# Kernel optimization log

Measured on AMD Instinct MI355X. Metric: run time of the kernel, lower is better.

The kernel has to match this reference:

```python
import jax, jax.numpy as jnp
import numpy as np

T, B, OBS, H, A = 512, 64, 512, 1024, 18


def setup_inputs() -> dict:
    key = jax.random.key(0)
    ks = jax.random.split(key, 8)
    s = lambda fan: 1.0 / np.sqrt(fan)
    return {
        "obs": jax.random.normal(ks[0], (T, B, OBS), jnp.float32),
        # binary done/valid mask per (timestep, env)
        "mask": (jax.random.uniform(ks[1], (T, B)) > 0.05).astype(jnp.float32),
        "W_enc": jax.random.normal(ks[2], (H, OBS), jnp.float32) * s(OBS),
        "b_enc": jnp.zeros((H,), jnp.float32),
        "W_ih": jax.random.normal(ks[3], (4 * H, H), jnp.float32) * s(H),
        "b_ih": jnp.zeros((4 * H,), jnp.float32),
        "W_hh": jax.random.normal(ks[4], (4 * H, H), jnp.float32) * s(H),
        "b_hh": jnp.zeros((4 * H,), jnp.float32),
        "W_dec": jax.random.normal(ks[5], (A, H), jnp.float32) * s(H),
        "b_dec": jnp.zeros((A,), jnp.float32),
    }


def reference(obs, mask, W_enc, b_enc, W_ih, b_ih, W_hh, b_hh, W_dec, b_dec):
    # encoder MLP + relu, batched over all T*B (one big GEMM)
    encoded = jax.nn.relu(jnp.einsum("tbo,ho->tbh", obs, W_enc) + b_enc)
    # precompute input contribution to LSTM gates for all timesteps: [T,B,4H]
    x_gates = jnp.einsum("tbh,gh->tbg", encoded, W_ih) + b_ih + b_hh

    def step(carry, inp):
        h, c = carry
        xg, m = inp  # xg: [B,4H], m: [B]
        gates = xg + h @ W_hh.T
        i, f, g, o = jnp.split(gates, 4, axis=-1)  # torch LSTMCell order
        c_new = jax.nn.sigmoid(f) * c + jax.nn.sigmoid(i) * jnp.tanh(g)
        h_new = jax.nn.sigmoid(o) * jnp.tanh(c_new)
        m = m[:, None]
        h_new = h_new * m
        c_new = c_new * m
        return (h_new, c_new), h_new

    h0 = jnp.zeros((B, H), jnp.float32)
    c0 = jnp.zeros((B, H), jnp.float32)
    (h, c), latent = jax.lax.scan(step, (h0, c0), (x_gates, mask))

    # decoder over flattened (T*B, H) then mask q-values
    values = jnp.einsum("tbh,ah->tba", latent, W_dec) + b_dec
    values = values * mask[..., None]
    return values, h, c
```

## Files before the change

kernel.cpp:

```cpp
#include <hip/hip_runtime.h>
#include <hip/hip_bf16.h>

#define T_ 512
#define B_ 64
#define OBS_ 512
#define H_ 1024
#define A_ 18
#define MM_ (T_*B_)
#define G4_ (4*H_)
#define CH_ 64
#define NCH_ (T_/CH_)
#define CM_ (CH_*B_)
#define NG_ 256

typedef unsigned short u16;
typedef unsigned long long u64;
typedef __attribute__((ext_vector_type(8))) short s8v;
typedef __attribute__((ext_vector_type(4))) float f4v;

__device__ __forceinline__ float b2f(u16 u){
    unsigned x = ((unsigned)u) << 16;
    return __builtin_bit_cast(float, x);
}
__device__ __forceinline__ u16 f2b(float f){
    unsigned x = __builtin_bit_cast(unsigned, f);
    return (u16)((x + 0x7fffu + ((x >> 16) & 1u)) >> 16);
}


__global__ void cast_f32_bf16(const float* __restrict__ in, u16* __restrict__ out, int n){
    int i = blockIdx.x * blockDim.x + threadIdx.x;
    int stride = gridDim.x * blockDim.x;
    for (; i < n; i += stride) out[i] = f2b(in[i]);
}

__global__ void add_bias2(const float* __restrict__ a, const float* __restrict__ b,
                          float* __restrict__ out, int n){
    int i = blockIdx.x * blockDim.x + threadIdx.x;
    if (i < n) out[i] = a[i] + b[i];
}

__global__ void init_scan(u16* __restrict__ h_hist, float* __restrict__ c,
                          unsigned* __restrict__ flags){
    int i = blockIdx.x * blockDim.x + threadIdx.x;
    int stride = gridDim.x * blockDim.x;
    unsigned* h0 = (unsigned*)h_hist;
    for (int k = i; k < B_*H_/2; k += stride) h0[k] = 0u;
    for (int k = i; k < B_*H_; k += stride) c[k] = 0.f;
    if (i < 512) flags[i] = 0u;
}

__global__ void copy_hc(const float* __restrict__ h, const float* __restrict__ c,
                        float* __restrict__ out){
    int i = blockIdx.x * blockDim.x + threadIdx.x;
    out[(size_t)MM_*A_ + i] = h[i];
    out[(size_t)MM_*A_ + B_*H_ + i] = c[i];
}


#define LDSS 72

template<bool A_FP32, bool RELU>
__global__ __launch_bounds__(256) void gemm_bt(
    const void* __restrict__ Aptr, const u16* __restrict__ W,
    const float* __restrict__ bias, u16* __restrict__ C,
    int M, int N, int K)
{
    __shared__ __align__(16) u16 As[128 * LDSS];
    __shared__ __align__(16) u16 Bs[128 * LDSS];

    const int tid  = threadIdx.x;
    const int lane = tid & 63;
    const int wid  = tid >> 6;
    const int wm   = wid & 1, wn = wid >> 1;
    const int m0   = blockIdx.y * 128, n0 = blockIdx.x * 128;
    const int quad = lane >> 4, l16 = lane & 15;

    f4v acc[4][4];
    #pragma unroll
    for (int i = 0; i < 4; i++)
        #pragma unroll
        for (int j = 0; j < 4; j++) acc[i][j] = (f4v){0.f,0.f,0.f,0.f};

    for (int k0 = 0; k0 < K; k0 += 64){
        __syncthreads();
        if (A_FP32){
            const float* A = (const float*)Aptr;
            #pragma unroll
            for (int pss = 0; pss < 8; pss++){
                int idx = pss * 256 + tid;
                int row = idx >> 4, ch = idx & 15;
                float4 v = *(const float4*)(A + (size_t)(m0 + row) * K + k0 + ch * 4);
                u16* d = &As[row * LDSS + ch * 4];
                d[0] = f2b(v.x); d[1] = f2b(v.y); d[2] = f2b(v.z); d[3] = f2b(v.w);
            }
        } else {
            const u16* A = (const u16*)Aptr;
            #pragma unroll
            for (int pss = 0; pss < 4; pss++){
                int idx = pss * 256 + tid;
                int row = idx >> 3, ch = idx & 7;
                *(uint4*)&As[row * LDSS + ch * 8] =
                    *(const uint4*)(A + (size_t)(m0 + row) * K + k0 + ch * 8);
            }
        }
        #pragma unroll
        for (int pss = 0; pss < 4; pss++){
            int idx = pss * 256 + tid;
            int row = idx >> 3, ch = idx & 7;
            *(uint4*)&Bs[row * LDSS + ch * 8] =
                *(const uint4*)(W + (size_t)(n0 + row) * K + k0 + ch * 8);
        }
        __syncthreads();

        #pragma unroll
        for (int kk = 0; kk < 64; kk += 32){
            s8v af[4], bf[4];
            #pragma unroll
            for (int mt = 0; mt < 4; mt++)
                af[mt] = *(const s8v*)&As[(wm*64 + mt*16 + l16) * LDSS + kk + quad*8];
            #pragma unroll
            for (int nt = 0; nt < 4; nt++)
                bf[nt] = *(const s8v*)&Bs[(wn*64 + nt*16 + l16) * LDSS + kk + quad*8];
            #pragma unroll
            for (int mt = 0; mt < 4; mt++)
                #pragma unroll
                for (int nt = 0; nt < 4; nt++)
                    acc[mt][nt] = __builtin_amdgcn_mfma_f32_16x16x32_bf16(
                        af[mt], bf[nt], acc[mt][nt], 0, 0, 0);
        }
    }

    #pragma unroll
    for (int mt = 0; mt < 4; mt++){
        #pragma unroll
        for (int nt = 0; nt < 4; nt++){
            #pragma unroll
            for (int r = 0; r < 4; r++){
                int m = m0 + wm*64 + mt*16 + quad*4 + r;
                int n = n0 + wn*64 + nt*16 + l16;
                float v = acc[mt][nt][r] + bias[n];
                if (RELU) v = fmaxf(v, 0.f);
                C[(size_t)m * N + n] = f2b(v);
            }
        }
    }
}


__global__ __launch_bounds__(256, 1) void fused_scan_gemm(
    const u16* __restrict__ xg,
    const u16* __restrict__ Whh,
    u16* __restrict__ h_hist,
    float* __restrict__ c_glob,
    float* __restrict__ h_f32,
    const float* __restrict__ mask,
    unsigned* __restrict__ flags,
    int t0,
    const u16* __restrict__ encA,
    const u16* __restrict__ Wih,
    const float* __restrict__ bias2,
    u16* __restrict__ xg_next,
    int ntiles)
{
    __shared__ __align__(16) char smem[2 * 128 * LDSS * 2];

    const int tid  = threadIdx.x;
    const int lane = tid & 63;
    const int w    = tid >> 6;
    const int quad = lane >> 4, l16 = lane & 15;

    if (blockIdx.x >= 256){
        if (ntiles == 0) return;
        u16* As = (u16*)smem;
        u16* Bs = As + 128 * LDSS;
        const int wm = w & 1, wn = w >> 1;

        for (int tile = (int)blockIdx.x - 256; tile < ntiles; tile += NG_){
            const int n0 = (tile & 31) * 128;
            const int m0 = (tile >> 5) * 128;

            f4v acc[4][4];
            #pragma unroll
            for (int i = 0; i < 4; i++)
                #pragma unroll
                for (int j = 0; j < 4; j++) acc[i][j] = (f4v){0.f,0.f,0.f,0.f};

            for (int k0 = 0; k0 < H_; k0 += 64){
                __syncthreads();
                #pragma unroll
                for (int pss = 0; pss < 4; pss++){
                    int idx = pss * 256 + tid;
                    int row = idx >> 3, ch = idx & 7;
                    *(uint4*)&As[row * LDSS + ch * 8] =
                        *(const uint4*)(encA + (size_t)(m0 + row) * H_ + k0 + ch * 8);
                    *(uint4*)&Bs[row * LDSS + ch * 8] =
                        *(const uint4*)(Wih + (size_t)(n0 + row) * H_ + k0 + ch * 8);
                }
                __syncthreads();

                #pragma unroll
                for (int kk = 0; kk < 64; kk += 32){
                    s8v af[4], bf[4];
                    #pragma unroll
                    for (int mt = 0; mt < 4; mt++)
                        af[mt] = *(const s8v*)&As[(wm*64 + mt*16 + l16) * LDSS + kk + quad*8];
                    #pragma unroll
                    for (int nt = 0; nt < 4; nt++)
                        bf[nt] = *(const s8v*)&Bs[(wn*64 + nt*16 + l16) * LDSS + kk + quad*8];
                    #pragma unroll
                    for (int mt = 0; mt < 4; mt++)
                        #pragma unroll
                        for (int nt = 0; nt < 4; nt++)
                            acc[mt][nt] = __builtin_amdgcn_mfma_f32_16x16x32_bf16(
                                af[mt], bf[nt], acc[mt][nt], 0, 0, 0);
                }
            }
            __syncthreads();

            #pragma unroll
            for (int mt = 0; mt < 4; mt++){
                #pragma unroll
                for (int nt = 0; nt < 4; nt++){
                    #pragma unroll
                    for (int r = 0; r < 4; r++){
                        int m = m0 + wm*64 + mt*16 + quad*4 + r;
                        int n = n0 + wn*64 + nt*16 + l16;
                        xg_next[(size_t)m * G4_ + n] = f2b(acc[mt][nt][r] + bias2[n]);
                    }
                }
            }
        }
        return;
    }

    float (*red)[4][16][17] = (float(*)[4][16][17])smem;

    const int bid  = blockIdx.x;
    const int g = bid & 3, s = bid >> 2;
    const int rb0 = g * 16, j0 = s * 16;

    const int koff = w * 256;
    s8v bf[4][8];
    #pragma unroll
    for (int gate = 0; gate < 4; gate++)
        #pragma unroll
        for (int ks = 0; ks < 8; ks++)
            bf[gate][ks] = *(const s8v*)(
                Whh + (size_t)(gate * H_ + j0 + l16) * H_ + koff + ks * 32 + quad * 8);

    const int cb = tid >> 4, cu = tid & 15;
    const size_t cidx = (size_t)(rb0 + cb) * H_ + j0 + cu;
    float c_reg = c_glob[cidx];

    const size_t hoff = (size_t)(rb0 + l16) * H_ + koff + quad * 8;

    unsigned* myflag = flags + ((g * 4 + (s >> 4)) << 5) + (s & 15);
    const unsigned* pollp = flags + ((g * 4 + w) << 5) + l16;

    const u16* xg0 = xg + (size_t)(rb0 + cb) * G4_ + j0 + cu;
    u16 nxi = xg0[0], nxf = xg0[H_], nxv = xg0[2 * H_], nxo = xg0[3 * H_];
    float nm = mask[rb0 + cb];

    for (int st = 0; st < CH_; st++){
        const float xi = b2f(nxi), xf = b2f(nxf), xv = b2f(nxv), xo = b2f(nxo);
        const float m = nm;

        const unsigned tgt = (unsigned)(t0 + st);
        int tries = 0;
        for (;;){
            unsigned f = __hip_atomic_load(pollp, __ATOMIC_RELAXED, __HIP_MEMORY_SCOPE_AGENT);
            if (__all((int)(f >= tgt))) break;
            if (++tries > (1 << 20)) break;
            if (tries >= 8) __builtin_amdgcn_s_sleep(1);
        }

        const u16* hs = h_hist + (size_t)st * B_ * H_ + hoff;
        f4v acc[4];
        #pragma unroll
        for (int gate = 0; gate < 4; gate++) acc[gate] = (f4v){0.f,0.f,0.f,0.f};
        #pragma unroll
        for (int ks = 0; ks < 8; ks++){
            s8v af = *(const s8v*)(hs + ks * 32);
            #pragma unroll
            for (int gate = 0; gate < 4; gate++)
                acc[gate] = __builtin_amdgcn_mfma_f32_16x16x32_bf16(af, bf[gate][ks], acc[gate], 0, 0, 0);
        }
        #pragma unroll
        for (int gate = 0; gate < 4; gate++)
            #pragma unroll
            for (int r = 0; r < 4; r++)
                red[w][gate][quad * 4 + r][l16] = acc[gate][r];
        __syncthreads();

        float gi = xi, gf = xf, gg = xv, go = xo;
        #pragma unroll
        for (int ww = 0; ww < 4; ww++){
            gi += red[ww][0][cb][cu];
            gf += red[ww][1][cb][cu];
            gg += red[ww][2][cb][cu];
            go += red[ww][3][cb][cu];
        }

        float is = 1.f / (1.f + __expf(-gi));
        float fs = 1.f / (1.f + __expf(-gf));
        float os = 1.f / (1.f + __expf(-go));
        float gt = tanhf(gg);

        float cn = fs * c_reg + is * gt;
        float hn = os * tanhf(cn);
        hn *= m; cn *= m;
        c_reg = cn;
        if (t0 + st == T_ - 1) h_f32[cidx] = hn;

        unsigned hb = (unsigned)f2b(hn);
        unsigned partner = (unsigned)__shfl_xor((int)hb, 1, 64);
        if ((cu & 1) == 0){
            unsigned packed = hb | (partner << 16);
            unsigned* dst = (unsigned*)(h_hist + (size_t)(st + 1) * B_ * H_ + cidx);
            __hip_atomic_store(dst, packed, __ATOMIC_RELAXED, __HIP_MEMORY_SCOPE_AGENT);
            if (st == CH_ - 1){
                unsigned* dst0 = (unsigned*)(h_hist + cidx);
                __hip_atomic_store(dst0, packed, __ATOMIC_RELAXED, __HIP_MEMORY_SCOPE_AGENT);
            }
        }
        asm volatile("s_waitcnt vmcnt(0)" ::: "memory");
        __syncthreads();

        if (tid == 0)
            __hip_atomic_store(myflag, (unsigned)(t0 + st + 1),
                               __ATOMIC_RELAXED, __HIP_MEMORY_SCOPE_AGENT);

        if (st + 1 < CH_){
            const u16* xgn = xg + (size_t)(st + 1) * B_ * G4_ + (size_t)(rb0 + cb) * G4_ + j0 + cu;
            nxi = xgn[0]; nxf = xgn[H_]; nxv = xgn[2 * H_]; nxo = xgn[3 * H_];
            nm = mask[(size_t)(st + 1) * B_ + rb0 + cb];
        }
    }

    c_glob[cidx] = c_reg;
}


__global__ __launch_bounds__(256) void decode_kernel(
    const u16* __restrict__ latent, const u16* __restrict__ Wdec,
    const float* __restrict__ bdec, const float* __restrict__ mask,
    float* __restrict__ values, int rows)
{
    __shared__ __align__(16) u16 wl[A_ * H_];
    const int tid = threadIdx.x;
    for (int i = tid; i < A_ * H_ / 8; i += 256)
        ((uint4*)wl)[i] = ((const uint4*)Wdec)[i];
    __syncthreads();

    const int lane = tid & 63;
    int wid = blockIdx.x * 4 + (tid >> 6);
    const int nwaves = gridDim.x * 4;

    for (int row = wid; row < rows; row += nwaves){
        float lat[16];
        #pragma unroll
        for (int i = 0; i < 16; i++)
            lat[i] = b2f(latent[(size_t)row * H_ + i*64 + lane]);
        float acc[A_];
        #pragma unroll
        for (int a = 0; a < A_; a++) acc[a] = 0.f;
        #pragma unroll
        for (int i = 0; i < 16; i++){
            #pragma unroll
            for (int a = 0; a < A_; a++)
                acc[a] += lat[i] * b2f(wl[a * H_ + i*64 + lane]);
        }
        float m = mask[row];
        #pragma unroll
        for (int a = 0; a < A_; a++){
            float v = acc[a];
            #pragma unroll
            for (int s = 32; s > 0; s >>= 1) v += __shfl_down(v, s, 64);
            if (lane == 0) values[(size_t)row * A_ + a] = (v + bdec[a]) * m;
        }
    }
}


extern "C" void kernel_launch(void* const* d_in, const int* in_sizes, int n_in,
                              void* d_out, int out_size, void* d_ws, size_t ws_size,
                              hipStream_t stream)
{
    const float* obs  = (const float*)d_in[0];
    const float* mask = (const float*)d_in[1];
    const float* Wenc = (const float*)d_in[2];
    const float* benc = (const float*)d_in[3];
    const float* Wih  = (const float*)d_in[4];
    const float* bih  = (const float*)d_in[5];
    const float* Whh  = (const float*)d_in[6];
    const float* bhh  = (const float*)d_in[7];
    const float* Wdec = (const float*)d_in[8];
    const float* bdec = (const float*)d_in[9];
    float* out = (float*)d_out;

    char* p = (char*)d_ws;
    size_t o = 0;
    auto alloc = [&](size_t bytes){ void* r = p + o; o += (bytes + 255) & ~(size_t)255; return r; };
    u16*      wenc_b  = (u16*)     alloc((size_t)H_ * OBS_ * 2);
    u16*      wih_b   = (u16*)     alloc((size_t)G4_ * H_ * 2);
    u16*      whh_b   = (u16*)     alloc((size_t)G4_ * H_ * 2);
    u16*      wdec_b  = (u16*)     alloc((size_t)A_ * H_ * 2);
    float*    bias2   = (float*)   alloc((size_t)G4_ * 4);
    u16*      h_hist  = (u16*)     alloc((size_t)(CH_ + 1) * B_ * H_ * 2);
    float*    h_f32   = (float*)   alloc((size_t)B_ * H_ * 4);
    float*    c_f32   = (float*)   alloc((size_t)B_ * H_ * 4);
    unsigned* flags   = (unsigned*)alloc(512 * 4);

    const size_t enc_all_b = (size_t)MM_ * H_ * 2;
    const size_t xg_b      = (size_t)CM_ * G4_ * 2;
    const bool big = ws_size >= o + enc_all_b + 2 * xg_b + 4096;
    (void)in_sizes; (void)n_in; (void)out_size;

    cast_f32_bf16<<<1024, 256, 0, stream>>>(Wenc, wenc_b, H_ * OBS_);
    cast_f32_bf16<<<2048, 256, 0, stream>>>(Wih,  wih_b,  G4_ * H_);
    cast_f32_bf16<<<2048, 256, 0, stream>>>(Whh,  whh_b,  G4_ * H_);
    cast_f32_bf16<<<72,   256, 0, stream>>>(Wdec, wdec_b, A_ * H_);
    add_bias2<<<16, 256, 0, stream>>>(bih, bhh, bias2, G4_);
    init_scan<<<2048, 256, 0, stream>>>(h_hist, c_f32, flags);

    if (big){
        u16* enc_all = (u16*)alloc(enc_all_b);
        u16* xg_buf0 = (u16*)alloc(xg_b);
        u16* xg_buf1 = (u16*)alloc(xg_b);
        u16* xg_buf[2] = { xg_buf0, xg_buf1 };

        dim3 ge(H_ / 128, MM_ / 128);
        gemm_bt<true, true><<<ge, 256, 0, stream>>>(
            obs, wenc_b, benc, enc_all, MM_, H_, OBS_);

        dim3 gx(G4_ / 128, CM_ / 128);
        gemm_bt<false, false><<<gx, 256, 0, stream>>>(
            enc_all, wih_b, bias2, xg_buf[0], CM_, G4_, H_);

        for (int c = 0; c < NCH_; c++){
            const int t0 = c * CH_;
            const int nt = (c + 1 < NCH_) ? 1024 : 0;
            fused_scan_gemm<<<256 + NG_, 256, 0, stream>>>(
                xg_buf[c & 1], whh_b, h_hist, c_f32, h_f32,
                mask + (size_t)t0 * B_, flags, t0,
                enc_all + (size_t)(c + 1) * CM_ * H_, wih_b, bias2,
                xg_buf[(c + 1) & 1], nt);

            decode_kernel<<<256, 256, 0, stream>>>(
                h_hist + (size_t)B_ * H_, wdec_b, bdec, mask + (size_t)t0 * B_,
                out + (size_t)t0 * B_ * A_, CM_);
        }
    } else {
        u16* enc_ch = (u16*)alloc((size_t)CM_ * H_ * 2);
        u16* xg_ch  = (u16*)alloc(xg_b);

        for (int c = 0; c < NCH_; c++){
            const int t0 = c * CH_;

            dim3 g1(H_ / 128, CM_ / 128);
            gemm_bt<true, true><<<g1, 256, 0, stream>>>(
                obs + (size_t)t0 * B_ * OBS_, wenc_b, benc, enc_ch, CM_, H_, OBS_);

            dim3 g2(G4_ / 128, CM_ / 128);
            gemm_bt<false, false><<<g2, 256, 0, stream>>>(
                enc_ch, wih_b, bias2, xg_ch, CM_, G4_, H_);

            fused_scan_gemm<<<256, 256, 0, stream>>>(
                xg_ch, whh_b, h_hist, c_f32, h_f32,
                mask + (size_t)t0 * B_, flags, t0,
                (const u16*)nullptr, wih_b, bias2, (u16*)nullptr, 0);

            decode_kernel<<<256, 256, 0, stream>>>(
                h_hist + (size_t)B_ * H_, wdec_b, bdec, mask + (size_t)t0 * B_,
                out + (size_t)t0 * B_ * A_, CM_);
        }
    }

    copy_hc<<<256, 256, 0, stream>>>(h_f32, c_f32, out);
}
```

Baseline: 2.736 ms.

## Fuse previous-chunk decoder into scan kernel via double-buffered hidden history

The per-chunk decoder launch moves into the idle helper blocks of the fused scan kernel. They decode the previous chunk's hidden states, which now live in a second double-buffered h_hist, while the scan runs on the current chunk; only the final chunk is decoded by a separate launch. This aims to remove one kernel launch and its serialization per chunk and to hide decoder work behind the latency-bound scan. It also raises the scan blocks' wave priority, at the cost of extra workspace and more contention from helper blocks.

```diff
diff --git a/kernel.cpp b/kernel.cpp
--- a/kernel.cpp
+++ b/kernel.cpp
@@ -152,6 +152,7 @@
     const u16* __restrict__ xg,
     const u16* __restrict__ Whh,
     u16* __restrict__ h_hist,
+    u16* __restrict__ h_next,
     float* __restrict__ c_glob,
     float* __restrict__ h_f32,
     const float* __restrict__ mask,
@@ -161,7 +162,12 @@
     const u16* __restrict__ Wih,
     const float* __restrict__ bias2,
     u16* __restrict__ xg_next,
-    int ntiles)
+    int ntiles,
+    const u16* __restrict__ Wdec,
+    const float* __restrict__ bdec,
+    const u16* __restrict__ dec_latent,
+    const float* __restrict__ dec_mask,
+    float* __restrict__ dec_out)
 {
     __shared__ __align__(16) char smem[2 * 128 * LDSS * 2];
 
@@ -171,68 +177,104 @@
     const int quad = lane >> 4, l16 = lane & 15;
 
     if (blockIdx.x >= 256){
-        if (ntiles == 0) return;
-        u16* As = (u16*)smem;
-        u16* Bs = As + 128 * LDSS;
-        const int wm = w & 1, wn = w >> 1;
-
-        for (int tile = (int)blockIdx.x - 256; tile < ntiles; tile += NG_){
-            const int n0 = (tile & 31) * 128;
-            const int m0 = (tile >> 5) * 128;
-
-            f4v acc[4][4];
-            #pragma unroll
-            for (int i = 0; i < 4; i++)
-                #pragma unroll
-                for (int j = 0; j < 4; j++) acc[i][j] = (f4v){0.f,0.f,0.f,0.f};
-
-            for (int k0 = 0; k0 < H_; k0 += 64){
-                __syncthreads();
-                #pragma unroll
-                for (int pss = 0; pss < 4; pss++){
-                    int idx = pss * 256 + tid;
-                    int row = idx >> 3, ch = idx & 7;
-                    *(uint4*)&As[row * LDSS + ch * 8] =
-                        *(const uint4*)(encA + (size_t)(m0 + row) * H_ + k0 + ch * 8);
-                    *(uint4*)&Bs[row * LDSS + ch * 8] =
-                        *(const uint4*)(Wih + (size_t)(n0 + row) * H_ + k0 + ch * 8);
+        if (ntiles > 0){
+            u16* As = (u16*)smem;
+            u16* Bs = As + 128 * LDSS;
+            const int wm = w & 1, wn = w >> 1;
+
+            for (int tile = (int)blockIdx.x - 256; tile < ntiles; tile += NG_){
+                const int n0 = (tile & 31) * 128;
+                const int m0 = (tile >> 5) * 128;
+
+                f4v acc[4][4];
+                #pragma unroll
+                for (int i = 0; i < 4; i++)
+                    #pragma unroll
+                    for (int j = 0; j < 4; j++) acc[i][j] = (f4v){0.f,0.f,0.f,0.f};
+
+                for (int k0 = 0; k0 < H_; k0 += 64){
+                    __syncthreads();
+                    #pragma unroll
+                    for (int pss = 0; pss < 4; pss++){
+                        int idx = pss * 256 + tid;
+                        int row = idx >> 3, ch = idx & 7;
+                        *(uint4*)&As[row * LDSS + ch * 8] =
+                            *(const uint4*)(encA + (size_t)(m0 + row) * H_ + k0 + ch * 8);
+                        *(uint4*)&Bs[row * LDSS + ch * 8] =
+                            *(const uint4*)(Wih + (size_t)(n0 + row) * H_ + k0 + ch * 8);
+                    }
+                    __syncthreads();
+
+                    #pragma unroll
+                    for (int kk = 0; kk < 64; kk += 32){
+                        s8v af[4], bf[4];
+                        #pragma unroll
+                        for (int mt = 0; mt < 4; mt++)
+                            af[mt] = *(const s8v*)&As[(wm*64 + mt*16 + l16) * LDSS + kk + quad*8];
+                        #pragma unroll
+                        for (int nt = 0; nt < 4; nt++)
+                            bf[nt] = *(const s8v*)&Bs[(wn*64 + nt*16 + l16) * LDSS + kk + quad*8];
+                        #pragma unroll
+                        for (int mt = 0; mt < 4; mt++)
+                            #pragma unroll
+                            for (int nt = 0; nt < 4; nt++)
+                                acc[mt][nt] = __builtin_amdgcn_mfma_f32_16x16x32_bf16(
+                                    af[mt], bf[nt], acc[mt][nt], 0, 0, 0);
+                    }
                 }
                 __syncthreads();
 
                 #pragma unroll
-                for (int kk = 0; kk < 64; kk += 32){
-                    s8v af[4], bf[4];
+                for (int mt = 0; mt < 4; mt++){
                     #pragma unroll
-                    for (int mt = 0; mt < 4; mt++)
-                        af[mt] = *(const s8v*)&As[(wm*64 + mt*16 + l16) * LDSS + kk + quad*8];
-                    #pragma unroll
-                    for (int nt = 0; nt < 4; nt++)
-                        bf[nt] = *(const s8v*)&Bs[(wn*64 + nt*16 + l16) * LDSS + kk + quad*8];
-                    #pragma unroll
-                    for (int mt = 0; mt < 4; mt++)
+                    for (int nt = 0; nt < 4; nt++){
                         #pragma unroll
-                        for (int nt = 0; nt < 4; nt++)
-                            acc[mt][nt] = __builtin_amdgcn_mfma_f32_16x16x32_bf16(
-                                af[mt], bf[nt], acc[mt][nt], 0, 0, 0);
-                }
-            }
-            __syncthreads();
-
-            #pragma unroll
-            for (int mt = 0; mt < 4; mt++){
-                #pragma unroll
-                for (int nt = 0; nt < 4; nt++){
-                    #pragma unroll
-                    for (int r = 0; r < 4; r++){
-                        int m = m0 + wm*64 + mt*16 + quad*4 + r;
-                        int n = n0 + wn*64 + nt*16 + l16;
-                        xg_next[(size_t)m * G4_ + n] = f2b(acc[mt][nt][r] + bias2[n]);
+                        for (int r = 0; r < 4; r++){
+                            int m = m0 + wm*64 + mt*16 + quad*4 + r;
+                            int n = n0 + wn*64 + nt*16 + l16;
+                            xg_next[(size_t)m * G4_ + n] = f2b(acc[mt][nt][r] + bias2[n]);
+                        }
                     }
                 }
             }
         }
+
+        if (dec_latent){
+            __syncthreads();
+            u16* wl = (u16*)smem;
+            for (int i = tid; i < A_ * H_ / 8; i += 256)
+                ((uint4*)wl)[i] = ((const uint4*)Wdec)[i];
+            __syncthreads();
+
+            int wid = ((int)blockIdx.x - 256) * 4 + w;
+            for (int row = wid; row < CM_; row += NG_ * 4){
+                float lat[16];
+                #pragma unroll
+                for (int i = 0; i < 16; i++)
+                    lat[i] = b2f(dec_latent[(size_t)row * H_ + i*64 + lane]);
+                float dacc[A_];
+                #pragma unroll
+                for (int a = 0; a < A_; a++) dacc[a] = 0.f;
+                #pragma unroll
+                for (int i = 0; i < 16; i++){
+                    #pragma unroll
+                    for (int a = 0; a < A_; a++)
+                        dacc[a] += lat[i] * b2f(wl[a * H_ + i*64 + lane]);
+                }
+                float mm = dec_mask[row];
+                #pragma unroll
+                for (int a = 0; a < A_; a++){
+                    float v = dacc[a];
+                    #pragma unroll
+                    for (int sh = 32; sh > 0; sh >>= 1) v += __shfl_down(v, sh, 64);
+                    if (lane == 0) dec_out[(size_t)row * A_ + a] = (v + bdec[a]) * mm;
+                }
+            }
+        }
         return;
     }
+
+    __builtin_amdgcn_s_setprio(1);
 
     float (*red)[4][16][17] = (float(*)[4][16][17])smem;
 
@@ -320,7 +362,7 @@
             unsigned* dst = (unsigned*)(h_hist + (size_t)(st + 1) * B_ * H_ + cidx);
             __hip_atomic_store(dst, packed, __ATOMIC_RELAXED, __HIP_MEMORY_SCOPE_AGENT);
             if (st == CH_ - 1){
-                unsigned* dst0 = (unsigned*)(h_hist + cidx);
+                unsigned* dst0 = (unsigned*)(h_next + cidx);
                 __hip_atomic_store(dst0, packed, __ATOMIC_RELAXED, __HIP_MEMORY_SCOPE_AGENT);
             }
         }
@@ -407,14 +449,15 @@
     u16*      whh_b   = (u16*)     alloc((size_t)G4_ * H_ * 2);
     u16*      wdec_b  = (u16*)     alloc((size_t)A_ * H_ * 2);
     float*    bias2   = (float*)   alloc((size_t)G4_ * 4);
-    u16*      h_hist  = (u16*)     alloc((size_t)(CH_ + 1) * B_ * H_ * 2);
+    u16*      h_buf0  = (u16*)     alloc((size_t)(CH_ + 1) * B_ * H_ * 2);
     float*    h_f32   = (float*)   alloc((size_t)B_ * H_ * 4);
     float*    c_f32   = (float*)   alloc((size_t)B_ * H_ * 4);
     unsigned* flags   = (unsigned*)alloc(512 * 4);
 
+    const size_t hbuf_b    = (size_t)(CH_ + 1) * B_ * H_ * 2;
     const size_t enc_all_b = (size_t)MM_ * H_ * 2;
     const size_t xg_b      = (size_t)CM_ * G4_ * 2;
-    const bool big = ws_size >= o + enc_all_b + 2 * xg_b + 4096;
+    const bool big = ws_size >= o + hbuf_b + enc_all_b + 2 * xg_b + 4096;
     (void)in_sizes; (void)n_in; (void)out_size;
 
     cast_f32_bf16<<<1024, 256, 0, stream>>>(Wenc, wenc_b, H_ * OBS_);
@@ -422,13 +465,15 @@
     cast_f32_bf16<<<2048, 256, 0, stream>>>(Whh,  whh_b,  G4_ * H_);
     cast_f32_bf16<<<72,   256, 0, stream>>>(Wdec, wdec_b, A_ * H_);
     add_bias2<<<16, 256, 0, stream>>>(bih, bhh, bias2, G4_);
-    init_scan<<<2048, 256, 0, stream>>>(h_hist, c_f32, flags);
+    init_scan<<<2048, 256, 0, stream>>>(h_buf0, c_f32, flags);
 
     if (big){
+        u16* h_buf1  = (u16*)alloc(hbuf_b);
         u16* enc_all = (u16*)alloc(enc_all_b);
         u16* xg_buf0 = (u16*)alloc(xg_b);
         u16* xg_buf1 = (u16*)alloc(xg_b);
         u16* xg_buf[2] = { xg_buf0, xg_buf1 };
+        u16* h_buf[2]  = { h_buf0, h_buf1 };
 
         dim3 ge(H_ / 128, MM_ / 128);
         gemm_bt<true, true><<<ge, 256, 0, stream>>>(
@@ -441,16 +486,22 @@
         for (int c = 0; c < NCH_; c++){
             const int t0 = c * CH_;
             const int nt = (c + 1 < NCH_) ? 1024 : 0;
+            const u16*  dlat = (c > 0) ? h_buf[(c - 1) & 1] + (size_t)B_ * H_ : nullptr;
+            const float* dmk = (c > 0) ? mask + (size_t)(c - 1) * CH_ * B_ : mask;
+            float*      dout = (c > 0) ? out + (size_t)(c - 1) * CM_ * A_ : out;
+
             fused_scan_gemm<<<256 + NG_, 256, 0, stream>>>(
-                xg_buf[c & 1], whh_b, h_hist, c_f32, h_f32,
-                mask + (size_t)t0 * B_, flags, t0,
-                enc_all + (size_t)(c + 1) * CM_ * H_, wih_b, bias2,
-                xg_buf[(c + 1) & 1], nt);
-
-            decode_kernel<<<256, 256, 0, stream>>>(
-                h_hist + (size_t)B_ * H_, wdec_b, bdec, mask + (size_t)t0 * B_,
-                out + (size_t)t0 * B_ * A_, CM_);
-        }
+                xg_buf[c & 1], whh_b, h_buf[c & 1], h_buf[(c + 1) & 1],
+                c_f32, h_f32, mask + (size_t)t0 * B_, flags, t0,
+                enc_all + (size_t)(c + 1 < NCH_ ? c + 1 : 0) * CM_ * H_,
+                wih_b, bias2, xg_buf[(c + 1) & 1], nt,
+                wdec_b, bdec, dlat, dmk, dout);
+        }
+
+        decode_kernel<<<256, 256, 0, stream>>>(
+            h_buf[(NCH_ - 1) & 1] + (size_t)B_ * H_, wdec_b, bdec,
+            mask + (size_t)(NCH_ - 1) * CH_ * B_,
+            out + (size_t)(NCH_ - 1) * CM_ * A_, CM_);
     } else {
         u16* enc_ch = (u16*)alloc((size_t)CM_ * H_ * 2);
         u16* xg_ch  = (u16*)alloc(xg_b);
@@ -467,12 +518,13 @@
                 enc_ch, wih_b, bias2, xg_ch, CM_, G4_, H_);
 
             fused_scan_gemm<<<256, 256, 0, stream>>>(
-                xg_ch, whh_b, h_hist, c_f32, h_f32,
+                xg_ch, whh_b, h_buf0, h_buf0, c_f32, h_f32,
                 mask + (size_t)t0 * B_, flags, t0,
-                (const u16*)nullptr, wih_b, bias2, (u16*)nullptr, 0);
+                (const u16*)nullptr, wih_b, bias2, (u16*)nullptr, 0,
+                wdec_b, bdec, (const u16*)nullptr, mask, out);
 
             decode_kernel<<<256, 256, 0, stream>>>(
-                h_hist + (size_t)B_ * H_, wdec_b, bdec, mask + (size_t)t0 * B_,
+                h_buf0 + (size_t)B_ * H_, wdec_b, bdec, mask + (size_t)t0 * B_,
                 out + (size_t)t0 * B_ * A_, CM_);
         }
     }
```

Measured after the change: 2.857 ms. 4.4% more time.
